# Kernel optimization log

Hardware: AMD Instinct MI355X
Metric: run time of the kernel (lower is better)

## Reference

```python
import jax, jax.numpy as jnp
import numpy as np

N_NODES = 50000
N_ADJS = 6
N_EDGES = 800000
N_HID_PREV = 256
N_HID = 256
N_STEP = 3
LN_EPS = 1e-5


def _spmm(rows, cols, vals, x, n_nodes):
    # sparse [N,N] @ dense [N,D]: gather source rows, scale by edge value, scatter-add to dest
    return jax.ops.segment_sum(vals[:, None] * x[cols], rows, num_segments=n_nodes)


def _layernorm(x, gamma, beta):
    mu = jnp.mean(x, axis=-1, keepdims=True)
    var = jnp.var(x, axis=-1, keepdims=True)
    return (x - mu) * jax.lax.rsqrt(var + LN_EPS) * gamma + beta


def setup_inputs() -> dict:
    key = jax.random.key(0)
    ks = jax.random.split(key, 8)
    x = jax.random.normal(ks[0], (N_NODES, N_HID_PREV), dtype=jnp.float32)
    adj_rows = jax.random.randint(ks[1], (N_ADJS, N_EDGES), 0, N_NODES, dtype=jnp.int32)
    adj_cols = jax.random.randint(ks[2], (N_ADJS, N_EDGES), 0, N_NODES, dtype=jnp.int32)
    # scale values ~1/avg_degree so repeated aggregation stays numerically tame
    adj_vals = jax.random.uniform(ks[3], (N_ADJS, N_EDGES), dtype=jnp.float32) / 16.0
    idxes_seq = jax.random.randint(ks[4], (N_STEP,), 0, N_ADJS, dtype=jnp.int64)
    idxes_res = jax.random.randint(ks[5], (N_STEP * (N_STEP - 1) // 2,), 0, N_ADJS, dtype=jnp.int64)
    W = jax.random.normal(ks[6], (N_HID, N_HID_PREV), dtype=jnp.float32) * (1.0 / np.sqrt(N_HID_PREV))
    b = jnp.zeros((N_HID,), dtype=jnp.float32)
    gamma = jnp.ones((N_HID,), dtype=jnp.float32)
    beta = jnp.zeros((N_HID,), dtype=jnp.float32)
    return {"x": x, "adj_rows": adj_rows, "adj_cols": adj_cols, "adj_vals": adj_vals,
            "idxes_seq": idxes_seq, "idxes_res": idxes_res, "W": W, "b": b,
            "gamma": gamma, "beta": beta, "connection_dict": 0}


def reference(x, adj_rows, adj_cols, adj_vals, idxes_seq, idxes_res, W, b, gamma, beta, connection_dict):
    n_nodes = x.shape[0]
    h = x @ W.T + b  # affine
    states = [h]
    offset = 0
    for i in range(N_STEP):
        si = idxes_seq[i]
        seqi = _spmm(adj_rows[si], adj_cols[si], adj_vals[si], states[i], n_nodes)
        resi = jnp.zeros_like(seqi)
        for j in range(i):
            ri = idxes_res[offset + j]
            resi = resi + _spmm(adj_rows[ri], adj_cols[ri], adj_vals[ri], states[j], n_nodes)
        offset += i
        states.append(seqi + resi)
    out = _layernorm(states[-1], gamma, beta)
    return jax.nn.gelu(out, approximate=False)  # torch F.gelu default is exact erf
```

## Files before the change

### kernel.cpp

```cpp
#include <hip/hip_runtime.h>
#include <math.h>

#define N_NODES 50000
#define N_EDGES 800000
#define N_ADJS  6
#define NHID    256
#define BSHIFT  7
#define NB      391
#define SLOTCAP 2560
#define BCAP    2816
#define LN_EPS  1e-5f

typedef _Float16 f16x8 __attribute__((ext_vector_type(8)));
typedef float f32x4  __attribute__((ext_vector_type(4)));
typedef _Float16 h4  __attribute__((ext_vector_type(4)));

__global__ __launch_bounds__(256) void convert_w(const float* __restrict__ W,
                                                 _Float16* __restrict__ Wh)
{
    const int i = blockIdx.x * 256 + threadIdx.x;
    Wh[i] = (_Float16)W[i];
}

__global__ __launch_bounds__(256) void gemm_mfma(const float* __restrict__ x,
                                                 const _Float16* __restrict__ Wh,
                                                 const float* __restrict__ bias,
                                                 _Float16* __restrict__ h)
{
    const int tid = threadIdx.x;
    const int w = tid >> 6, l = tid & 63;
    const int m = l & 15, q = l >> 4;
    const int row0 = blockIdx.x * 64 + w * 16;
    const int arow = row0 + m;
    const int arow_c = (arow < N_NODES) ? arow : 0;

    f32x4 acc[16];
    #pragma unroll
    for (int nt = 0; nt < 16; ++nt) acc[nt] = (f32x4){0.f, 0.f, 0.f, 0.f};

    for (int kt = 0; kt < NHID; kt += 32) {
        const float* xp = x + (size_t)arow_c * NHID + kt + q * 8;
        const float4 xa = *(const float4*)xp;
        const float4 xb = *(const float4*)(xp + 4);
        f16x8 ah;
        ah[0] = (_Float16)xa.x; ah[1] = (_Float16)xa.y;
        ah[2] = (_Float16)xa.z; ah[3] = (_Float16)xa.w;
        ah[4] = (_Float16)xb.x; ah[5] = (_Float16)xb.y;
        ah[6] = (_Float16)xb.z; ah[7] = (_Float16)xb.w;
        const int ko = kt + q * 8;
        #pragma unroll
        for (int nt = 0; nt < 16; ++nt) {
            const size_t off = (size_t)(nt * 16 + m) * NHID + ko;
            const f16x8 bh = *(const f16x8*)(Wh + off);
            acc[nt] = __builtin_amdgcn_mfma_f32_16x16x32_f16(ah, bh, acc[nt], 0, 0, 0);
        }
    }

    #pragma unroll
    for (int nt = 0; nt < 16; ++nt) {
        const int col = nt * 16 + m;
        const float bv = bias[col];
        #pragma unroll
        for (int r = 0; r < 4; ++r) {
            const int grow = row0 + q * 4 + r;
            if (grow < N_NODES) h[(size_t)grow * NHID + col] = (_Float16)(acc[nt][r] + bv);
        }
    }
}

__global__ __launch_bounds__(256) void bucket_scatter(const int* __restrict__ rows_all,
                                                      const int* __restrict__ cols_all,
                                                      const float* __restrict__ vals_all,
                                                      int* __restrict__ gcnt,
                                                      int2* __restrict__ slots)
{
    const int a = blockIdx.y;
    __shared__ int lcnt[NB], lbase[NB];
    for (int i = threadIdx.x; i < NB; i += 256) lcnt[i] = 0;
    __syncthreads();
    int bq[16], sq[16]; int2 pq[16];
    const int e0 = blockIdx.x * 4096 + threadIdx.x;
    #pragma unroll
    for (int j = 0; j < 16; ++j) {
        const int e = e0 + j * 256;
        bq[j] = -1;
        if (e < N_EDGES) {
            const size_t idx = (size_t)a * N_EDGES + e;
            const int r = rows_all[idx];
            const int b = r >> BSHIFT;
            bq[j] = b;
            sq[j] = atomicAdd(&lcnt[b], 1);
            pq[j].x = (r << 16) | cols_all[idx];
            pq[j].y = __float_as_int(vals_all[idx]);
        }
    }
    __syncthreads();
    for (int i = threadIdx.x; i < NB; i += 256)
        lbase[i] = lcnt[i] ? atomicAdd(&gcnt[a * NB + i], lcnt[i]) : 0;
    __syncthreads();
    #pragma unroll
    for (int j = 0; j < 16; ++j)
        if (bq[j] >= 0)
            slots[((size_t)a * NB + bq[j]) * SLOTCAP + lbase[bq[j]] + sq[j]] = pq[j];
}

__global__ __launch_bounds__(384) void scan_buckets(const int* __restrict__ gcnt,
                                                    int* __restrict__ bstart,
                                                    int* __restrict__ row_start)
{
    const int lane = threadIdx.x & 63, a = threadIdx.x >> 6;
    if (a >= N_ADJS) return;
    int carry = 0;
    #pragma unroll
    for (int c = 0; c < 7; ++c) {
        const int i = c * 64 + lane;
        const int v = (i < NB) ? gcnt[a * NB + i] : 0;
        int xs = v;
        #pragma unroll
        for (int d = 1; d < 64; d <<= 1) { const int t = __shfl_up(xs, d, 64); if (lane >= d) xs += t; }
        const int excl = carry + xs - v;
        if (i < NB) bstart[a * (NB + 1) + i] = excl;
        carry += __shfl(xs, 63, 64);
    }
    if (lane == 0) {
        bstart[a * (NB + 1) + NB] = N_EDGES;
        row_start[(size_t)a * (N_NODES + 1) + N_NODES] = N_EDGES;
    }
}

__global__ __launch_bounds__(256) void build_csr(const int2* __restrict__ slots,
                                                 const int* __restrict__ bstart,
                                                 int* __restrict__ row_start,
                                                 int2* __restrict__ sorted_cv)
{
    const int a = blockIdx.y, b = blockIdx.x;
    const int s = bstart[a * (NB + 1) + b];
    const int n = bstart[a * (NB + 1) + b + 1] - s;
    __shared__ int cnt[128], cur[128];
    __shared__ int2 buf[BCAP];
    __shared__ int2 buf2[BCAP];
    if (threadIdx.x < 128) cnt[threadIdx.x] = 0;
    __syncthreads();
    const int2* bk = slots + ((size_t)a * NB + b) * SLOTCAP;
    const bool fits = (n <= BCAP);
    for (int i = threadIdx.x; i < n; i += 256) {
        const int2 p = bk[i];
        if (fits) buf[i] = p;
        atomicAdd(&cnt[(p.x >> 16) & 127], 1);
    }
    __syncthreads();
    const int lane = threadIdx.x & 63, wid = threadIdx.x >> 6;
    if (wid == 0) {
        const int i0 = lane * 2;
        const int c0 = cnt[i0], c1 = cnt[i0 + 1];
        const int sum = c0 + c1;
        int xs = sum;
        #pragma unroll
        for (int d = 1; d < 64; d <<= 1) { const int t = __shfl_up(xs, d, 64); if (lane >= d) xs += t; }
        const int base = xs - sum;
        const int o0 = base, o1 = base + c0;
        cur[i0] = o0; cur[i0 + 1] = o1;
        int* rs = row_start + (size_t)a * (N_NODES + 1);
        const int gr = (b << BSHIFT) + i0;
        if (gr + 0 < N_NODES) rs[gr + 0] = s + o0;
        if (gr + 1 < N_NODES) rs[gr + 1] = s + o1;
    }
    __syncthreads();
    int2* sc = sorted_cv + (size_t)a * N_EDGES;
    if (fits) {
        for (int i = threadIdx.x; i < n; i += 256) {
            const int2 p = buf[i];
            const int pos = atomicAdd(&cur[(p.x >> 16) & 127], 1);
            int2 cv; cv.x = p.x & 0xFFFF; cv.y = p.y;
            buf2[pos] = cv;
        }
        __syncthreads();
        for (int i = threadIdx.x; i < n; i += 256)
            sc[s + i] = buf2[i];
    } else {
        for (int i = threadIdx.x; i < n; i += 256) {
            const int2 p = bk[i];
            const int pos = atomicAdd(&cur[(p.x >> 16) & 127], 1);
            int2 cv; cv.x = p.x & 0xFFFF; cv.y = p.y;
            sc[s + pos] = cv;
        }
    }
}

static __device__ __forceinline__ void gacc(const _Float16* __restrict__ src,
                                            int col, float v, int lane, f32x4& acc)
{
    const h4 g = *(const h4*)(src + (size_t)col * NHID + lane * 4);
    acc[0] += v * (float)g[0];
    acc[1] += v * (float)g[1];
    acc[2] += v * (float)g[2];
    acc[3] += v * (float)g[3];
}

static __device__ __forceinline__ void pull_part(const int* __restrict__ row_start,
                                                 const int2* __restrict__ sorted_cv,
                                                 int a, const _Float16* __restrict__ src,
                                                 int row, int lane, f32x4& acc)
{
    const int2* cv = sorted_cv + (size_t)a * N_EDGES;
    const int* rs  = row_start + (size_t)a * (N_NODES + 1);
    const int s = rs[row], epnd = rs[row + 1];
    int e = s;
    for (; e + 3 < epnd; e += 4) {
        const int2 p0 = cv[e];
        const int2 p1 = cv[e + 1];
        const int2 p2 = cv[e + 2];
        const int2 p3 = cv[e + 3];
        gacc(src, p0.x, __int_as_float(p0.y), lane, acc);
        gacc(src, p1.x, __int_as_float(p1.y), lane, acc);
        gacc(src, p2.x, __int_as_float(p2.y), lane, acc);
        gacc(src, p3.x, __int_as_float(p3.y), lane, acc);
    }
    for (; e < epnd; ++e) {
        const int2 p0 = cv[e];
        gacc(src, p0.x, __int_as_float(p0.y), lane, acc);
    }
}

template<int PARTS, bool LN>
__global__ __launch_bounds__(256) void pull_spmm(
    const int* __restrict__ row_start, const int2* __restrict__ sorted_cv,
    const int* __restrict__ idx_a, int pos_a, const _Float16* __restrict__ src_a,
    const int* __restrict__ idx_b, int pos_b, const _Float16* __restrict__ src_b,
    const int* __restrict__ idx_c, int pos_c, const _Float16* __restrict__ src_c,
    _Float16* __restrict__ outh, float* __restrict__ outf,
    const float* __restrict__ gamma, const float* __restrict__ beta)
{
    const int row  = (blockIdx.x * 256 + threadIdx.x) >> 6;
    const int lane = threadIdx.x & 63;
    if (row >= N_NODES) return;
    f32x4 acc = {0.f, 0.f, 0.f, 0.f};
    pull_part(row_start, sorted_cv, idx_a[pos_a], src_a, row, lane, acc);
    if constexpr (PARTS >= 2) pull_part(row_start, sorted_cv, idx_b[pos_b], src_b, row, lane, acc);
    if constexpr (PARTS >= 3) pull_part(row_start, sorted_cv, idx_c[pos_c], src_c, row, lane, acc);

    if constexpr (LN) {
        float sum = acc[0] + acc[1] + acc[2] + acc[3];
        float sq  = acc[0] * acc[0] + acc[1] * acc[1] + acc[2] * acc[2] + acc[3] * acc[3];
        #pragma unroll
        for (int off = 1; off < 64; off <<= 1) {
            sum += __shfl_xor(sum, off, 64);
            sq  += __shfl_xor(sq,  off, 64);
        }
        const float mu   = sum * (1.f / NHID);
        const float var  = sq * (1.f / NHID) - mu * mu;
        const float rstd = rsqrtf(var + LN_EPS);
        const float4 g4 = *(const float4*)(gamma + lane * 4);
        const float4 b4 = *(const float4*)(beta + lane * 4);
        const float g[4]  = {g4.x, g4.y, g4.z, g4.w};
        const float bb[4] = {b4.x, b4.y, b4.z, b4.w};
        f32x4 o;
        #pragma unroll
        for (int j = 0; j < 4; ++j) {
            const float y = (acc[j] - mu) * rstd * g[j] + bb[j];
            o[j] = 0.5f * y * (1.f + erff(y * 0.70710678118654752f));
        }
        __builtin_nontemporal_store(o, (f32x4*)(outf + (size_t)row * NHID + lane * 4));
    } else {
        h4 o;
        o[0] = (_Float16)acc[0]; o[1] = (_Float16)acc[1];
        o[2] = (_Float16)acc[2]; o[3] = (_Float16)acc[3];
        __builtin_nontemporal_store(o, (h4*)(outh + (size_t)row * NHID + lane * 4));
    }
}

extern "C" void kernel_launch(void* const* d_in, const int* in_sizes, int n_in,
                              void* d_out, int out_size, void* d_ws, size_t ws_size,
                              hipStream_t stream)
{
    (void)in_sizes; (void)n_in; (void)out_size; (void)ws_size;
    const float* x        = (const float*)d_in[0];
    const int* adj_rows   = (const int*)d_in[1];
    const int* adj_cols   = (const int*)d_in[2];
    const float* vals     = (const float*)d_in[3];
    const int* idx_seq    = (const int*)d_in[4];
    const int* idx_res    = (const int*)d_in[5];
    const float* W        = (const float*)d_in[6];
    const float* bias     = (const float*)d_in[7];
    const float* gam      = (const float*)d_in[8];
    const float* bet      = (const float*)d_in[9];

    const size_t S = (size_t)N_NODES * NHID;
    _Float16* s0 = (_Float16*)d_ws;
    _Float16* s1 = s0 + S;
    _Float16* s2 = s1 + S;
    int2*  sorted_cv      = (int2*)(s2 + S);
    int*   row_start      = (int*)(sorted_cv + (size_t)N_ADJS * N_EDGES);
    _Float16* Wh          = (_Float16*)(row_start + (size_t)N_ADJS * (N_NODES + 1));
    int*   gcnt           = (int*)(Wh + NHID * NHID);
    int*   bstart         = gcnt + N_ADJS * NB;
    int2*  slots          = (int2*)s1;

    hipMemsetAsync(gcnt, 0, (size_t)N_ADJS * NB * sizeof(int), stream);

    convert_w<<<dim3(NHID * NHID / 256), dim3(256), 0, stream>>>(W, Wh);
    gemm_mfma<<<dim3((N_NODES + 63) / 64), dim3(256), 0, stream>>>(x, Wh, bias, s0);

    const int eblocks = (N_EDGES + 4095) / 4096;
    bucket_scatter<<<dim3(eblocks, N_ADJS), dim3(256), 0, stream>>>(adj_rows, adj_cols, vals, gcnt, slots);
    scan_buckets<<<dim3(1), dim3(384), 0, stream>>>(gcnt, bstart, row_start);
    build_csr<<<dim3(NB, N_ADJS), dim3(256), 0, stream>>>(slots, bstart, row_start, sorted_cv);

    const dim3 pgrid(N_NODES * 64 / 256);
    pull_spmm<1, false><<<pgrid, dim3(256), 0, stream>>>(row_start, sorted_cv,
        idx_seq, 0, s0,  nullptr, 0, nullptr,  nullptr, 0, nullptr,
        s1, nullptr, nullptr, nullptr);
    pull_spmm<2, false><<<pgrid, dim3(256), 0, stream>>>(row_start, sorted_cv,
        idx_seq, 1, s1,  idx_res, 0, s0,  nullptr, 0, nullptr,
        s2, nullptr, nullptr, nullptr);
    pull_spmm<3, true><<<pgrid, dim3(256), 0, stream>>>(row_start, sorted_cv,
        idx_seq, 2, s2,  idx_res, 1, s0,  idx_res, 2, s1,
        nullptr, (float*)d_out, gam, bet);
}
```

Measured before the change: 658.7 us.

## Stage bucket scatter in LDS and make pull SpMM waves own row ranges per phase

After: 680.9 us. 3.4% more time.

```diff
diff --git a/kernel.cpp b/kernel.cpp
--- a/kernel.cpp
+++ b/kernel.cpp
@@ -9,6 +9,10 @@
 #define NB      391
 #define SLOTCAP 2560
 #define BCAP    2816
+#define EPB     2048
+#define PULL_BLOCKS 1536
+#define PULL_WAVES  (PULL_BLOCKS * 4)
+#define RMAX    9
 #define LN_EPS  1e-5f
 
 typedef _Float16 f16x8 __attribute__((ext_vector_type(8)));
@@ -75,33 +79,55 @@
                                                       int2* __restrict__ slots)
 {
     const int a = blockIdx.y;
-    __shared__ int lcnt[NB], lbase[NB];
+    __shared__ int2 buf[EPB];
+    __shared__ int2 buf2[EPB];
+    __shared__ int lcnt[NB], lscan[NB], lcur[NB], lbase[NB];
     for (int i = threadIdx.x; i < NB; i += 256) lcnt[i] = 0;
     __syncthreads();
-    int bq[16], sq[16]; int2 pq[16];
-    const int e0 = blockIdx.x * 4096 + threadIdx.x;
-    #pragma unroll
-    for (int j = 0; j < 16; ++j) {
-        const int e = e0 + j * 256;
-        bq[j] = -1;
-        if (e < N_EDGES) {
-            const size_t idx = (size_t)a * N_EDGES + e;
-            const int r = rows_all[idx];
-            const int b = r >> BSHIFT;
-            bq[j] = b;
-            sq[j] = atomicAdd(&lcnt[b], 1);
-            pq[j].x = (r << 16) | cols_all[idx];
-            pq[j].y = __float_as_int(vals_all[idx]);
-        }
-    }
-    __syncthreads();
-    for (int i = threadIdx.x; i < NB; i += 256)
-        lbase[i] = lcnt[i] ? atomicAdd(&gcnt[a * NB + i], lcnt[i]) : 0;
-    __syncthreads();
-    #pragma unroll
-    for (int j = 0; j < 16; ++j)
-        if (bq[j] >= 0)
-            slots[((size_t)a * NB + bq[j]) * SLOTCAP + lbase[bq[j]] + sq[j]] = pq[j];
+    const int e0 = blockIdx.x * EPB;
+    const int n = min(EPB, N_EDGES - e0);
+    for (int i = threadIdx.x; i < n; i += 256) {
+        const size_t idx = (size_t)a * N_EDGES + e0 + i;
+        const int r = rows_all[idx];
+        int2 pq;
+        pq.x = (r << 16) | cols_all[idx];
+        pq.y = __float_as_int(vals_all[idx]);
+        buf[i] = pq;
+        atomicAdd(&lcnt[r >> BSHIFT], 1);
+    }
+    __syncthreads();
+    if (threadIdx.x < 64) {
+        const int lane = threadIdx.x;
+        int carry = 0;
+        #pragma unroll
+        for (int c = 0; c < 7; ++c) {
+            const int i = c * 64 + lane;
+            const int v = (i < NB) ? lcnt[i] : 0;
+            int xs = v;
+            #pragma unroll
+            for (int d = 1; d < 64; d <<= 1) { const int t = __shfl_up(xs, d, 64); if (lane >= d) xs += t; }
+            const int excl = carry + xs - v;
+            if (i < NB) {
+                lscan[i] = excl; lcur[i] = excl;
+                lbase[i] = v ? atomicAdd(&gcnt[a * NB + i], v) : 0;
+            }
+            carry += __shfl(xs, 63, 64);
+        }
+    }
+    __syncthreads();
+    for (int i = threadIdx.x; i < n; i += 256) {
+        const int2 p = buf[i];
+        const unsigned r = ((unsigned)p.x) >> 16;
+        const int pos = atomicAdd(&lcur[r >> BSHIFT], 1);
+        buf2[pos] = p;
+    }
+    __syncthreads();
+    for (int i = threadIdx.x; i < n; i += 256) {
+        const int2 p = buf2[i];
+        const unsigned r = ((unsigned)p.x) >> 16;
+        const int b = r >> BSHIFT;
+        slots[((size_t)a * NB + b) * SLOTCAP + lbase[b] + (i - lscan[b])] = p;
+    }
 }
 
 __global__ __launch_bounds__(384) void scan_buckets(const int* __restrict__ gcnt,
@@ -223,7 +249,7 @@
 }
 
 template<int PARTS, bool LN>
-__global__ __launch_bounds__(256) void pull_spmm(
+__global__ __launch_bounds__(256, 6) void pull_phased(
     const int* __restrict__ row_start, const int2* __restrict__ sorted_cv,
     const int* __restrict__ idx_a, int pos_a, const _Float16* __restrict__ src_a,
     const int* __restrict__ idx_b, int pos_b, const _Float16* __restrict__ src_b,
@@ -231,41 +257,73 @@
     _Float16* __restrict__ outh, float* __restrict__ outf,
     const float* __restrict__ gamma, const float* __restrict__ beta)
 {
-    const int row  = (blockIdx.x * 256 + threadIdx.x) >> 6;
+    const int wave = blockIdx.x * 4 + (threadIdx.x >> 6);
     const int lane = threadIdx.x & 63;
-    if (row >= N_NODES) return;
-    f32x4 acc = {0.f, 0.f, 0.f, 0.f};
-    pull_part(row_start, sorted_cv, idx_a[pos_a], src_a, row, lane, acc);
-    if constexpr (PARTS >= 2) pull_part(row_start, sorted_cv, idx_b[pos_b], src_b, row, lane, acc);
-    if constexpr (PARTS >= 3) pull_part(row_start, sorted_cv, idx_c[pos_c], src_c, row, lane, acc);
+    const int r0 = (int)((long long)wave * N_NODES / PULL_WAVES);
+    const int r1 = (int)((long long)(wave + 1) * N_NODES / PULL_WAVES);
+    const int nr = r1 - r0;
+
+    f32x4 acc[RMAX];
+    #pragma unroll
+    for (int k = 0; k < RMAX; ++k) acc[k] = (f32x4){0.f, 0.f, 0.f, 0.f};
+
+    {
+        const int a = idx_a[pos_a];
+        #pragma unroll
+        for (int k = 0; k < RMAX; ++k)
+            if (k < nr) pull_part(row_start, sorted_cv, a, src_a, r0 + k, lane, acc[k]);
+    }
+    if constexpr (PARTS >= 2) {
+        const int a = idx_b[pos_b];
+        #pragma unroll
+        for (int k = 0; k < RMAX; ++k)
+            if (k < nr) pull_part(row_start, sorted_cv, a, src_b, r0 + k, lane, acc[k]);
+    }
+    if constexpr (PARTS >= 3) {
+        const int a = idx_c[pos_c];
+        #pragma unroll
+        for (int k = 0; k < RMAX; ++k)
+            if (k < nr) pull_part(row_start, sorted_cv, a, src_c, r0 + k, lane, acc[k]);
+    }
 
     if constexpr (LN) {
-        float sum = acc[0] + acc[1] + acc[2] + acc[3];
-        float sq  = acc[0] * acc[0] + acc[1] * acc[1] + acc[2] * acc[2] + acc[3] * acc[3];
-        #pragma unroll
-        for (int off = 1; off < 64; off <<= 1) {
-            sum += __shfl_xor(sum, off, 64);
-            sq  += __shfl_xor(sq,  off, 64);
-        }
-        const float mu   = sum * (1.f / NHID);
-        const float var  = sq * (1.f / NHID) - mu * mu;
-        const float rstd = rsqrtf(var + LN_EPS);
         const float4 g4 = *(const float4*)(gamma + lane * 4);
         const float4 b4 = *(const float4*)(beta + lane * 4);
         const float g[4]  = {g4.x, g4.y, g4.z, g4.w};
         const float bb[4] = {b4.x, b4.y, b4.z, b4.w};
-        f32x4 o;
-        #pragma unroll
-        for (int j = 0; j < 4; ++j) {
-            const float y = (acc[j] - mu) * rstd * g[j] + bb[j];
-            o[j] = 0.5f * y * (1.f + erff(y * 0.70710678118654752f));
-        }
-        __builtin_nontemporal_store(o, (f32x4*)(outf + (size_t)row * NHID + lane * 4));
+        #pragma unroll
+        for (int k = 0; k < RMAX; ++k) {
+            if (k < nr) {
+                float sum = acc[k][0] + acc[k][1] + acc[k][2] + acc[k][3];
+                float sq  = acc[k][0]*acc[k][0] + acc[k][1]*acc[k][1]
+                          + acc[k][2]*acc[k][2] + acc[k][3]*acc[k][3];
+                #pragma unroll
+                for (int off = 1; off < 64; off <<= 1) {
+                    sum += __shfl_xor(sum, off, 64);
+                    sq  += __shfl_xor(sq,  off, 64);
+                }
+                const float mu   = sum * (1.f / NHID);
+                const float var  = sq * (1.f / NHID) - mu * mu;
+                const float rstd = rsqrtf(var + LN_EPS);
+                f32x4 o;
+                #pragma unroll
+                for (int j = 0; j < 4; ++j) {
+                    const float y = (acc[k][j] - mu) * rstd * g[j] + bb[j];
+                    o[j] = 0.5f * y * (1.f + erff(y * 0.70710678118654752f));
+                }
+                __builtin_nontemporal_store(o, (f32x4*)(outf + (size_t)(r0 + k) * NHID + lane * 4));
+            }
+        }
     } else {
-        h4 o;
-        o[0] = (_Float16)acc[0]; o[1] = (_Float16)acc[1];
-        o[2] = (_Float16)acc[2]; o[3] = (_Float16)acc[3];
-        __builtin_nontemporal_store(o, (h4*)(outh + (size_t)row * NHID + lane * 4));
+        #pragma unroll
+        for (int k = 0; k < RMAX; ++k) {
+            if (k < nr) {
+                h4 o;
+                o[0] = (_Float16)acc[k][0]; o[1] = (_Float16)acc[k][1];
+                o[2] = (_Float16)acc[k][2]; o[3] = (_Float16)acc[k][3];
+                __builtin_nontemporal_store(o, (h4*)(outh + (size_t)(r0 + k) * NHID + lane * 4));
+            }
+        }
     }
 }
 
@@ -301,19 +359,19 @@
     convert_w<<<dim3(NHID * NHID / 256), dim3(256), 0, stream>>>(W, Wh);
     gemm_mfma<<<dim3((N_NODES + 63) / 64), dim3(256), 0, stream>>>(x, Wh, bias, s0);
 
-    const int eblocks = (N_EDGES + 4095) / 4096;
+    const int eblocks = (N_EDGES + EPB - 1) / EPB;
     bucket_scatter<<<dim3(eblocks, N_ADJS), dim3(256), 0, stream>>>(adj_rows, adj_cols, vals, gcnt, slots);
     scan_buckets<<<dim3(1), dim3(384), 0, stream>>>(gcnt, bstart, row_start);
     build_csr<<<dim3(NB, N_ADJS), dim3(256), 0, stream>>>(slots, bstart, row_start, sorted_cv);
 
-    const dim3 pgrid(N_NODES * 64 / 256);
-    pull_spmm<1, false><<<pgrid, dim3(256), 0, stream>>>(row_start, sorted_cv,
+    const dim3 pgrid(PULL_BLOCKS);
+    pull_phased<1, false><<<pgrid, dim3(256), 0, stream>>>(row_start, sorted_cv,
         idx_seq, 0, s0,  nullptr, 0, nullptr,  nullptr, 0, nullptr,
         s1, nullptr, nullptr, nullptr);
-    pull_spmm<2, false><<<pgrid, dim3(256), 0, stream>>>(row_start, sorted_cv,
+    pull_phased<2, false><<<pgrid, dim3(256), 0, stream>>>(row_start, sorted_cv,
         idx_seq, 1, s1,  idx_res, 0, s0,  nullptr, 0, nullptr,
         s2, nullptr, nullptr, nullptr);
-    pull_spmm<3, true><<<pgrid, dim3(256), 0, stream>>>(row_start, sorted_cv,
+    pull_phased<3, true><<<pgrid, dim3(256), 0, stream>>>(row_start, sorted_cv,
         idx_seq, 2, s2,  idx_res, 1, s0,  idx_res, 2, s1,
         nullptr, (float*)d_out, gam, bet);
 }
```

## Coalesce bucket scatter via LDS sort, drop scan kernel using atomic bucket cursors

Applied to the files above, without the earlier changes.

After: 672.3 us. +2.1%, slower.

```diff
diff --git a/kernel.cpp b/kernel.cpp
--- a/kernel.cpp
+++ b/kernel.cpp
@@ -9,6 +9,8 @@
 #define NB      391
 #define SLOTCAP 2560
 #define BCAP    2816
+#define EPB     3072
+#define GPAD    16
 #define LN_EPS  1e-5f
 
 typedef _Float16 f16x8 __attribute__((ext_vector_type(8)));
@@ -16,10 +18,14 @@
 typedef _Float16 h4  __attribute__((ext_vector_type(4)));
 
 __global__ __launch_bounds__(256) void convert_w(const float* __restrict__ W,
-                                                 _Float16* __restrict__ Wh)
+                                                 _Float16* __restrict__ Wh,
+                                                 int* __restrict__ gcnt,
+                                                 int* __restrict__ cursor)
 {
     const int i = blockIdx.x * 256 + threadIdx.x;
     Wh[i] = (_Float16)W[i];
+    if (i < N_ADJS * NB) gcnt[i * GPAD] = 0;
+    if (i < N_ADJS) cursor[i * GPAD] = 0;
 }
 
 __global__ __launch_bounds__(256) void gemm_mfma(const float* __restrict__ x,
@@ -75,71 +81,72 @@
                                                       int2* __restrict__ slots)
 {
     const int a = blockIdx.y;
-    __shared__ int lcnt[NB], lbase[NB];
+    __shared__ int2 buf[EPB];
+    __shared__ int2 buf2[EPB];
+    __shared__ int lcnt[NB], lscan[NB], lcur[NB], lbase[NB];
     for (int i = threadIdx.x; i < NB; i += 256) lcnt[i] = 0;
     __syncthreads();
-    int bq[16], sq[16]; int2 pq[16];
-    const int e0 = blockIdx.x * 4096 + threadIdx.x;
-    #pragma unroll
-    for (int j = 0; j < 16; ++j) {
-        const int e = e0 + j * 256;
-        bq[j] = -1;
-        if (e < N_EDGES) {
-            const size_t idx = (size_t)a * N_EDGES + e;
-            const int r = rows_all[idx];
-            const int b = r >> BSHIFT;
-            bq[j] = b;
-            sq[j] = atomicAdd(&lcnt[b], 1);
-            pq[j].x = (r << 16) | cols_all[idx];
-            pq[j].y = __float_as_int(vals_all[idx]);
-        }
-    }
-    __syncthreads();
-    for (int i = threadIdx.x; i < NB; i += 256)
-        lbase[i] = lcnt[i] ? atomicAdd(&gcnt[a * NB + i], lcnt[i]) : 0;
-    __syncthreads();
-    #pragma unroll
-    for (int j = 0; j < 16; ++j)
-        if (bq[j] >= 0)
-            slots[((size_t)a * NB + bq[j]) * SLOTCAP + lbase[bq[j]] + sq[j]] = pq[j];
-}
-
-__global__ __launch_bounds__(384) void scan_buckets(const int* __restrict__ gcnt,
-                                                    int* __restrict__ bstart,
-                                                    int* __restrict__ row_start)
-{
-    const int lane = threadIdx.x & 63, a = threadIdx.x >> 6;
-    if (a >= N_ADJS) return;
-    int carry = 0;
-    #pragma unroll
-    for (int c = 0; c < 7; ++c) {
-        const int i = c * 64 + lane;
-        const int v = (i < NB) ? gcnt[a * NB + i] : 0;
-        int xs = v;
-        #pragma unroll
-        for (int d = 1; d < 64; d <<= 1) { const int t = __shfl_up(xs, d, 64); if (lane >= d) xs += t; }
-        const int excl = carry + xs - v;
-        if (i < NB) bstart[a * (NB + 1) + i] = excl;
-        carry += __shfl(xs, 63, 64);
-    }
-    if (lane == 0) {
-        bstart[a * (NB + 1) + NB] = N_EDGES;
-        row_start[(size_t)a * (N_NODES + 1) + N_NODES] = N_EDGES;
+    const int e0 = blockIdx.x * EPB;
+    const int n = min(EPB, N_EDGES - e0);
+    for (int i = threadIdx.x; i < n; i += 256) {
+        const size_t idx = (size_t)a * N_EDGES + e0 + i;
+        const int r = rows_all[idx];
+        int2 pq;
+        pq.x = (r << 16) | cols_all[idx];
+        pq.y = __float_as_int(vals_all[idx]);
+        buf[i] = pq;
+        atomicAdd(&lcnt[r >> BSHIFT], 1);
+    }
+    __syncthreads();
+    if (threadIdx.x < 64) {
+        const int lane = threadIdx.x;
+        int carry = 0;
+        #pragma unroll
+        for (int c = 0; c < 7; ++c) {
+            const int i = c * 64 + lane;
+            const int v = (i < NB) ? lcnt[i] : 0;
+            int xs = v;
+            #pragma unroll
+            for (int d = 1; d < 64; d <<= 1) { const int t = __shfl_up(xs, d, 64); if (lane >= d) xs += t; }
+            const int excl = carry + xs - v;
+            if (i < NB) {
+                lscan[i] = excl; lcur[i] = excl;
+                lbase[i] = v ? atomicAdd(&gcnt[(a * NB + i) * GPAD], v) : 0;
+            }
+            carry += __shfl(xs, 63, 64);
+        }
+    }
+    __syncthreads();
+    for (int i = threadIdx.x; i < n; i += 256) {
+        const int2 p = buf[i];
+        const unsigned r = ((unsigned)p.x) >> 16;
+        const int pos = atomicAdd(&lcur[r >> BSHIFT], 1);
+        buf2[pos] = p;
+    }
+    __syncthreads();
+    for (int i = threadIdx.x; i < n; i += 256) {
+        const int2 p = buf2[i];
+        const unsigned r = ((unsigned)p.x) >> 16;
+        const int b = r >> BSHIFT;
+        slots[((size_t)a * NB + b) * SLOTCAP + lbase[b] + (i - lscan[b])] = p;
     }
 }
 
 __global__ __launch_bounds__(256) void build_csr(const int2* __restrict__ slots,
-                                                 const int* __restrict__ bstart,
-                                                 int* __restrict__ row_start,
+                                                 const int* __restrict__ gcnt,
+                                                 int* __restrict__ cursor,
+                                                 int* __restrict__ rs_start,
+                                                 int* __restrict__ rs_cnt,
                                                  int2* __restrict__ sorted_cv)
 {
     const int a = blockIdx.y, b = blockIdx.x;
-    const int s = bstart[a * (NB + 1) + b];
-    const int n = bstart[a * (NB + 1) + b + 1] - s;
+    const int n = gcnt[(a * NB + b) * GPAD];
     __shared__ int cnt[128], cur[128];
+    __shared__ int s_base;
     __shared__ int2 buf[BCAP];
     __shared__ int2 buf2[BCAP];
     if (threadIdx.x < 128) cnt[threadIdx.x] = 0;
+    if (threadIdx.x == 0) s_base = atomicAdd(&cursor[a * GPAD], n);
     __syncthreads();
     const int2* bk = slots + ((size_t)a * NB + b) * SLOTCAP;
     const bool fits = (n <= BCAP);
@@ -149,6 +156,7 @@
         atomicAdd(&cnt[(p.x >> 16) & 127], 1);
     }
     __syncthreads();
+    const int s = s_base;
     const int lane = threadIdx.x & 63, wid = threadIdx.x >> 6;
     if (wid == 0) {
         const int i0 = lane * 2;
@@ -160,10 +168,11 @@
         const int base = xs - sum;
         const int o0 = base, o1 = base + c0;
         cur[i0] = o0; cur[i0 + 1] = o1;
-        int* rs = row_start + (size_t)a * (N_NODES + 1);
+        int* rsS = rs_start + (size_t)a * N_NODES;
+        int* rsC = rs_cnt   + (size_t)a * N_NODES;
         const int gr = (b << BSHIFT) + i0;
-        if (gr + 0 < N_NODES) rs[gr + 0] = s + o0;
-        if (gr + 1 < N_NODES) rs[gr + 1] = s + o1;
+        if (gr + 0 < N_NODES) { rsS[gr + 0] = s + o0; rsC[gr + 0] = c0; }
+        if (gr + 1 < N_NODES) { rsS[gr + 1] = s + o1; rsC[gr + 1] = c1; }
     }
     __syncthreads();
     int2* sc = sorted_cv + (size_t)a * N_EDGES;
@@ -197,14 +206,15 @@
     acc[3] += v * (float)g[3];
 }
 
-static __device__ __forceinline__ void pull_part(const int* __restrict__ row_start,
+static __device__ __forceinline__ void pull_part(const int* __restrict__ rs_start,
+                                                 const int* __restrict__ rs_cnt,
                                                  const int2* __restrict__ sorted_cv,
                                                  int a, const _Float16* __restrict__ src,
                                                  int row, int lane, f32x4& acc)
 {
     const int2* cv = sorted_cv + (size_t)a * N_EDGES;
-    const int* rs  = row_start + (size_t)a * (N_NODES + 1);
-    const int s = rs[row], epnd = rs[row + 1];
+    const int s    = rs_start[(size_t)a * N_NODES + row];
+    const int epnd = s + rs_cnt[(size_t)a * N_NODES + row];
     int e = s;
     for (; e + 3 < epnd; e += 4) {
         const int2 p0 = cv[e];
@@ -224,7 +234,8 @@
 
 template<int PARTS, bool LN>
 __global__ __launch_bounds__(256) void pull_spmm(
-    const int* __restrict__ row_start, const int2* __restrict__ sorted_cv,
+    const int* __restrict__ rs_start, const int* __restrict__ rs_cnt,
+    const int2* __restrict__ sorted_cv,
     const int* __restrict__ idx_a, int pos_a, const _Float16* __restrict__ src_a,
     const int* __restrict__ idx_b, int pos_b, const _Float16* __restrict__ src_b,
     const int* __restrict__ idx_c, int pos_c, const _Float16* __restrict__ src_c,
@@ -235,9 +246,9 @@
     const int lane = threadIdx.x & 63;
     if (row >= N_NODES) return;
     f32x4 acc = {0.f, 0.f, 0.f, 0.f};
-    pull_part(row_start, sorted_cv, idx_a[pos_a], src_a, row, lane, acc);
-    if constexpr (PARTS >= 2) pull_part(row_start, sorted_cv, idx_b[pos_b], src_b, row, lane, acc);
-    if constexpr (PARTS >= 3) pull_part(row_start, sorted_cv, idx_c[pos_c], src_c, row, lane, acc);
+    pull_part(rs_start, rs_cnt, sorted_cv, idx_a[pos_a], src_a, row, lane, acc);
+    if constexpr (PARTS >= 2) pull_part(rs_start, rs_cnt, sorted_cv, idx_b[pos_b], src_b, row, lane, acc);
+    if constexpr (PARTS >= 3) pull_part(rs_start, rs_cnt, sorted_cv, idx_c[pos_c], src_c, row, lane, acc);
 
     if constexpr (LN) {
         float sum = acc[0] + acc[1] + acc[2] + acc[3];
@@ -290,30 +301,28 @@
     _Float16* s1 = s0 + S;
     _Float16* s2 = s1 + S;
     int2*  sorted_cv      = (int2*)(s2 + S);
-    int*   row_start      = (int*)(sorted_cv + (size_t)N_ADJS * N_EDGES);
-    _Float16* Wh          = (_Float16*)(row_start + (size_t)N_ADJS * (N_NODES + 1));
+    int*   rs_start       = (int*)(sorted_cv + (size_t)N_ADJS * N_EDGES);
+    int*   rs_cnt         = rs_start + (size_t)N_ADJS * N_NODES;
+    _Float16* Wh          = (_Float16*)(rs_cnt + (size_t)N_ADJS * N_NODES);
     int*   gcnt           = (int*)(Wh + NHID * NHID);
-    int*   bstart         = gcnt + N_ADJS * NB;
+    int*   cursor         = gcnt + N_ADJS * NB * GPAD;
     int2*  slots          = (int2*)s1;
 
-    hipMemsetAsync(gcnt, 0, (size_t)N_ADJS * NB * sizeof(int), stream);
-
-    convert_w<<<dim3(NHID * NHID / 256), dim3(256), 0, stream>>>(W, Wh);
+    convert_w<<<dim3(NHID * NHID / 256), dim3(256), 0, stream>>>(W, Wh, gcnt, cursor);
     gemm_mfma<<<dim3((N_NODES + 63) / 64), dim3(256), 0, stream>>>(x, Wh, bias, s0);
 
-    const int eblocks = (N_EDGES + 4095) / 4096;
+    const int eblocks = (N_EDGES + EPB - 1) / EPB;
     bucket_scatter<<<dim3(eblocks, N_ADJS), dim3(256), 0, stream>>>(adj_rows, adj_cols, vals, gcnt, slots);
-    scan_buckets<<<dim3(1), dim3(384), 0, stream>>>(gcnt, bstart, row_start);
-    build_csr<<<dim3(NB, N_ADJS), dim3(256), 0, stream>>>(slots, bstart, row_start, sorted_cv);
+    build_csr<<<dim3(NB, N_ADJS), dim3(256), 0, stream>>>(slots, gcnt, cursor, rs_start, rs_cnt, sorted_cv);
 
     const dim3 pgrid(N_NODES * 64 / 256);
-    pull_spmm<1, false><<<pgrid, dim3(256), 0, stream>>>(row_start, sorted_cv,
+    pull_spmm<1, false><<<pgrid, dim3(256), 0, stream>>>(rs_start, rs_cnt, sorted_cv,
         idx_seq, 0, s0,  nullptr, 0, nullptr,  nullptr, 0, nullptr,
         s1, nullptr, nullptr, nullptr);
-    pull_spmm<2, false><<<pgrid, dim3(256), 0, stream>>>(row_start, sorted_cv,
+    pull_spmm<2, false><<<pgrid, dim3(256), 0, stream>>>(rs_start, rs_cnt, sorted_cv,
         idx_seq, 1, s1,  idx_res, 0, s0,  nullptr, 0, nullptr,
         s2, nullptr, nullptr, nullptr);
-    pull_spmm<3, true><<<pgrid, dim3(256), 0, stream>>>(row_start, sorted_cv,
+    pull_spmm<3, true><<<pgrid, dim3(256), 0, stream>>>(rs_start, rs_cnt, sorted_cv,
         idx_seq, 2, s2,  idx_res, 1, s0,  idx_res, 2, s1,
         nullptr, (float*)d_out, gam, bet);
 }
```
